# Kernel tuning notes

Hardware: AMD Instinct MI355X
Metric: run time of the kernel (lower is better)

The kernel has to match this reference:

```python
import jax, jax.numpy as jnp
import numpy as np
from jax import lax

D_MODEL, D_STATE, D_CONV, D_INNER, DT_RANK = 1024, 16, 4, 2048, 64
B_SZ, L_SEQ = 2, 4096

def setup_inputs() -> dict:
    key = jax.random.key(0)
    ks = jax.random.split(key, 12)
    s = 0.02
    x = jax.random.normal(ks[0], (B_SZ, L_SEQ, D_MODEL), jnp.float32)
    norm_w = jnp.ones((D_MODEL,), jnp.float32)
    norm_b = jnp.zeros((D_MODEL,), jnp.float32)
    W_in = jax.random.normal(ks[1], (D_MODEL, 2 * D_INNER), jnp.float32) * s
    conv_w = jax.random.normal(ks[2], (D_INNER, 1, D_CONV), jnp.float32) * 0.5
    conv_b = jnp.zeros((D_INNER,), jnp.float32)
    W_x = jax.random.normal(ks[3], (D_INNER, DT_RANK + 2 * D_STATE), jnp.float32) * s
    W_dt = jax.random.normal(ks[4], (DT_RANK, D_INNER), jnp.float32) * s
    # dt bias init as in the torch module: inverse-softplus of dt in [dt_min, dt_max]
    dt_init = jnp.exp(jax.random.uniform(ks[5], (D_INNER,)) * (np.log(0.1) - np.log(0.001)) + np.log(0.001))
    dt_init = jnp.clip(dt_init, 1e-4, None)
    b_dt = dt_init + jnp.log(-jnp.expm1(-dt_init))
    A_log = jnp.log(jnp.broadcast_to(jnp.arange(1, D_STATE + 1, dtype=jnp.float32)[None, :], (D_INNER, D_STATE)))
    D = jnp.ones((D_INNER,), jnp.float32)
    W_out = jax.random.normal(ks[6], (D_INNER, D_MODEL), jnp.float32) * s
    return {"x": x, "norm_w": norm_w, "norm_b": norm_b, "W_in": W_in,
            "conv_w": conv_w, "conv_b": conv_b, "W_x": W_x, "W_dt": W_dt,
            "b_dt": b_dt, "A_log": A_log, "D": D, "W_out": W_out}

def _silu(v):
    return v * jax.nn.sigmoid(v)

def _layernorm(v, w, b, eps=1e-5):
    mu = jnp.mean(v, axis=-1, keepdims=True)
    var = jnp.var(v, axis=-1, keepdims=True)
    return (v - mu) * lax.rsqrt(var + eps) * w + b

def _selective_scan(u, delta, A, Bm, Cm, Dp):
    # u, delta: [B,L,d_inner]; A: [d_inner,N]; Bm, Cm: [B,L,N]; Dp: [d_inner]
    Bb, L, d_inner = u.shape
    N = A.shape[1]

    def step(h, inp):
        dt_t, u_t, B_t, C_t = inp  # [B,d_inner],[B,d_inner],[B,N],[B,N]
        A_bar = jnp.exp(dt_t[..., None] * A)                       # [B,d_inner,N]
        h = A_bar * h + dt_t[..., None] * B_t[:, None, :] * u_t[..., None]
        y = jnp.sum(h * C_t[:, None, :], axis=-1)                  # [B,d_inner]
        return h, y

    h0 = jnp.zeros((Bb, d_inner, N), u.dtype)
    xs = (jnp.swapaxes(delta, 0, 1), jnp.swapaxes(u, 0, 1),
          jnp.swapaxes(Bm, 0, 1), jnp.swapaxes(Cm, 0, 1))
    _, ys = lax.scan(step, h0, xs)          # ys: [L,B,d_inner]
    y = jnp.swapaxes(ys, 0, 1)
    return y + u * Dp[None, None, :]

def reference(x, norm_w, norm_b, W_in, conv_w, conv_b, W_x, W_dt, b_dt, A_log, D, W_out):
    residual = x
    xn = _layernorm(x, norm_w, norm_b)
    xz = xn @ W_in                                      # [B,L,2*d_inner]
    x_ssm, z = jnp.split(xz, 2, axis=-1)
    # depthwise causal conv1d (torch pads both sides then truncates -> left pad)
    xt = jnp.swapaxes(x_ssm, 1, 2)                      # [B,d_inner,L]
    xt = jnp.pad(xt, ((0, 0), (0, 0), (D_CONV - 1, 0)))
    xc = lax.conv_general_dilated(xt, conv_w, window_strides=(1,), padding='VALID',
                                  feature_group_count=D_INNER,
                                  dimension_numbers=('NCH', 'OIH', 'NCH'))
    xc = xc + conv_b[None, :, None]
    x_conv = jnp.swapaxes(_silu(xc), 1, 2)              # [B,L,d_inner]
    x_dbl = x_conv @ W_x                                # [B,L,dt_rank+2N]
    dt_low, B_mat, C_mat = jnp.split(x_dbl, [DT_RANK, DT_RANK + D_STATE], axis=-1)
    delta = jax.nn.softplus(dt_low @ W_dt + b_dt)       # [B,L,d_inner]
    A = -jnp.exp(A_log)
    y = _selective_scan(x_conv, delta, A, B_mat, C_mat, D)
    y = y * _silu(z)
    return residual + y @ W_out
```

## Files before the change

### kernel.cpp

```cpp
#include <hip/hip_runtime.h>

typedef unsigned short u16;
typedef __attribute__((ext_vector_type(8))) __bf16 bf16x8;
typedef __attribute__((ext_vector_type(4))) float f32x4;

#define LSEQ 4096
#define DMODEL 1024
#define DINNER 2048

__device__ __forceinline__ float bf2f(u16 u) {
  union { unsigned u; float f; } v; v.u = ((unsigned)u) << 16; return v.f;
}
__device__ __forceinline__ u16 f2bf(float f) {
  union { float f; unsigned u; } v; v.f = f;
  unsigned r = v.u + 0x7fffu + ((v.u >> 16) & 1u);
  return (u16)(r >> 16);
}
__device__ __forceinline__ void gload_lds16(const void* g, void* l) {
  __builtin_amdgcn_global_load_lds(
      (__attribute__((address_space(1))) void*)(unsigned long long)g,
      (__attribute__((address_space(3))) void*)(unsigned int)(unsigned long long)l,
      16, 0, 0);
}
__device__ __forceinline__ float sigmoidf_(float v) { return 1.f / (1.f + __expf(-v)); }

__global__ __launch_bounds__(256) void ln_kernel(const float* __restrict__ x,
                                                 const float* __restrict__ w,
                                                 const float* __restrict__ b,
                                                 u16* __restrict__ out) {
  int row = blockIdx.x;
  const float* xr = x + (size_t)row * DMODEL;
  int t = threadIdx.x;
  float4 v = ((const float4*)xr)[t];
  float s = v.x + v.y + v.z + v.w;
  float s2 = v.x * v.x + v.y * v.y + v.z * v.z + v.w * v.w;
  for (int off = 32; off; off >>= 1) {
    s += __shfl_down(s, off);
    s2 += __shfl_down(s2, off);
  }
  __shared__ float ls[4], ls2[4];
  int wid = t >> 6;
  if ((t & 63) == 0) { ls[wid] = s; ls2[wid] = s2; }
  __syncthreads();
  s = ls[0] + ls[1] + ls[2] + ls[3];
  s2 = ls2[0] + ls2[1] + ls2[2] + ls2[3];
  float mu = s * (1.f / DMODEL);
  float var = s2 * (1.f / DMODEL) - mu * mu;
  float rs = rsqrtf(var + 1e-5f);
  float4 wv = ((const float4*)w)[t];
  float4 bv = ((const float4*)b)[t];
  unsigned p0 = (unsigned)f2bf((v.x - mu) * rs * wv.x + bv.x) |
                ((unsigned)f2bf((v.y - mu) * rs * wv.y + bv.y) << 16);
  unsigned p1 = (unsigned)f2bf((v.z - mu) * rs * wv.z + bv.z) |
                ((unsigned)f2bf((v.w - mu) * rs * wv.w + bv.w) << 16);
  ((uint2*)(out + (size_t)row * DMODEL))[t] = make_uint2(p0, p1);
}

__global__ __launch_bounds__(256) void tc_kernel(const float* __restrict__ in,
                                                 u16* __restrict__ out,
                                                 int K, int N, int Npad) {
  __shared__ float tile[32][33];
  int n0 = blockIdx.x * 32, k0 = blockIdx.y * 32;
  int tx = threadIdx.x & 31, ty = threadIdx.x >> 5;
  for (int i = ty; i < 32; i += 8) {
    int k = k0 + i, n = n0 + tx;
    tile[i][tx] = (k < K && n < N) ? in[(size_t)k * N + n] : 0.f;
  }
  __syncthreads();
  for (int i = ty; i < 32; i += 8) {
    int n = n0 + i, k = k0 + tx;
    if (n < Npad && k < K) out[(size_t)n * K + k] = f2bf(tile[tx][i]);
  }
}

__device__ __forceinline__ void stage8(const u16* grow0, int ld, int kcol0,
                                       u16* lds_u, int ln) {
  int rr = ln >> 3, kb = ln & 7;
  gload_lds16(grow0 + (size_t)rr * ld + kcol0 + ((kb ^ rr) << 3), lds_u);
}

#define LDA_FRAGS(mh, buf)                                                         \
  _Pragma("unroll") for (int mf = 0; mf < 4; ++mf)                                 \
  _Pragma("unroll") for (int kk = 0; kk < 2; ++kk)                                 \
    a[mf][kk] = *(const bf16x8*)(LA + (buf) * 16384 +                              \
        (wm * 128 + (mh) * 64 + mf * 16 + lr) * 64 + (((kk * 4 + lq) ^ key) << 3));

#define LDB_FRAGS(nh, buf)                                                         \
  _Pragma("unroll") for (int nf = 0; nf < 2; ++nf)                                 \
  _Pragma("unroll") for (int kk = 0; kk < 2; ++kk)                                 \
    bb[nh][nf][kk] = *(const bf16x8*)(LB + (buf) * 16384 +                         \
        (wn * 64 + (nh) * 32 + nf * 16 + lr) * 64 + (((kk * 4 + lq) ^ key) << 3));

#define MFMA_Q(mh, nh)                                                             \
  __builtin_amdgcn_s_setprio(1);                                                   \
  _Pragma("unroll") for (int mf = 0; mf < 4; ++mf)                                 \
  _Pragma("unroll") for (int nf = 0; nf < 2; ++nf)                                 \
  _Pragma("unroll") for (int kk = 0; kk < 2; ++kk)                                 \
    acc[(mh) * 4 + mf][(nh) * 2 + nf] = __builtin_amdgcn_mfma_f32_16x16x32_bf16(   \
        a[mf][kk], bb[nh][nf][kk], acc[(mh) * 4 + mf][(nh) * 2 + nf], 0, 0, 0);    \
  __builtin_amdgcn_s_setprio(0);

#define STAGE_A(unit, kt, buf)                                                     \
  _Pragma("unroll") for (int c = 0; c < 2; ++c) {                                  \
    int g = w * 2 + c;                                                             \
    int r0 = ((g < 8) ? g * 8 : (g - 8) * 8 + 128) + (unit) * 64;                  \
    stage8(Ag + (size_t)r0 * K, K, (kt) * 64, LA + (buf) * 16384 + r0 * 64, ln);   \
  }

#define STAGE_B(half, kt, buf)                                                     \
  _Pragma("unroll") for (int c = 0; c < 2; ++c) {                                  \
    int g = w * 2 + c;                                                             \
    int r0 = (g >> 2) * 64 + (half) * 32 + (g & 3) * 8;                            \
    stage8(Bg + (size_t)r0 * K, K, (kt) * 64, LB + (buf) * 16384 + r0 * 64, ln);   \
  }

template <int OUT_BF16, int EPI>
__global__ __launch_bounds__(512, 2) void gemm8p(const u16* __restrict__ A,
                                                 const u16* __restrict__ Bt,
                                                 void* __restrict__ Cout,
                                                 const float* __restrict__ aux,
                                                 int M, int N, int K, int cthresh) {
  __shared__ alignas(16) u16 lds[65536];
  u16* LA = lds;
  u16* LB = lds + 32768;
  int t = threadIdx.x;
  int w = t >> 6, ln = t & 63;
  int wm = w >> 2, wn = w & 3;
  int bm = blockIdx.y, bn = blockIdx.x;
  int lr = ln & 15, lq = ln >> 4, key = ln & 7;
  int NT = K >> 6;
  const u16* Ag = A + (size_t)bm * 256 * K;
  const u16* Bg = Bt + (size_t)bn * 256 * K;
  f32x4 acc[8][4] = {};
  bf16x8 a[4][2], bb[2][2][2];

  STAGE_A(0, 0, 0); STAGE_B(0, 0, 0); STAGE_B(1, 0, 0); STAGE_A(1, 0, 0);
  int k1 = NT > 1 ? 1 : 0;
  STAGE_A(0, k1, 1); STAGE_B(0, k1, 1); STAGE_B(1, k1, 1);
  asm volatile("s_waitcnt vmcnt(6)" ::: "memory");
  __builtin_amdgcn_s_barrier();

  for (int T = 0; T < NT; ++T) {
    int b0 = T & 1, b1 = b0 ^ 1;
    int kt1 = (T + 1 < NT) ? T + 1 : NT - 1;
    int kt2 = (T + 2 < NT) ? T + 2 : NT - 1;
    LDA_FRAGS(0, b0);
    LDB_FRAGS(0, b0);
    STAGE_A(1, kt1, b1);
    __builtin_amdgcn_s_barrier();
    asm volatile("s_waitcnt lgkmcnt(0)" ::: "memory");
    MFMA_Q(0, 0);
    __builtin_amdgcn_s_barrier();
    LDB_FRAGS(1, b0);
    STAGE_A(0, kt2, b0);
    __builtin_amdgcn_s_barrier();
    asm volatile("s_waitcnt lgkmcnt(0)" ::: "memory");
    MFMA_Q(0, 1);
    __builtin_amdgcn_s_barrier();
    LDA_FRAGS(1, b0);
    STAGE_B(0, kt2, b0);
    __builtin_amdgcn_s_barrier();
    asm volatile("s_waitcnt lgkmcnt(0)" ::: "memory");
    MFMA_Q(1, 1);
    __builtin_amdgcn_s_barrier();
    STAGE_B(1, kt2, b0);
    asm volatile("s_waitcnt vmcnt(6)" ::: "memory");
    __builtin_amdgcn_s_barrier();
    MFMA_Q(1, 0);
    __builtin_amdgcn_s_barrier();
  }

  int crow0 = bm * 256 + wm * 128;
  int ccol0 = bn * 256 + wn * 64;
#pragma unroll
  for (int mf = 0; mf < 8; ++mf)
#pragma unroll
    for (int nf = 0; nf < 4; ++nf)
#pragma unroll
      for (int r = 0; r < 4; ++r) {
        int row = crow0 + mf * 16 + lq * 4 + r;
        int col = ccol0 + nf * 16 + lr;
        float v = acc[mf][nf][r];
        if (EPI == 1) v += aux[(size_t)row * N + col];
        if (EPI == 2 && col >= cthresh) v = v * sigmoidf_(v);
        if (OUT_BF16)
          ((u16*)Cout)[(size_t)row * N + col] = f2bf(v);
        else
          ((float*)Cout)[(size_t)row * N + col] = v;
      }
}

template <int OUT_BF16, int EPI, int SPLITK>
__global__ __launch_bounds__(256) void gemm_bt(const u16* __restrict__ A,
                                               const u16* __restrict__ Bt,
                                               void* __restrict__ Cout,
                                               const float* __restrict__ aux,
                                               int M, int N, int K, int ld, int cthresh) {
  __shared__ alignas(16) u16 As[128 * 32];
  __shared__ alignas(16) u16 Bs[128 * 32];
  int t = threadIdx.x;
  int w = t >> 6, ln = t & 63;
  int wr = w >> 1, wc = w & 1;
  int bm = blockIdx.y, bn = blockIdx.x;
  int lr = ln & 15, lk = (ln >> 4) * 8;
  f32x4 acc[4][4] = {};
  int kz = SPLITK ? blockIdx.z * K : 0;
  const u16* Abase = A + (size_t)bm * 128 * ld + kz;
  const u16* Bbase = Bt + (size_t)bn * 128 * ld + kz;
  for (int k0 = 0; k0 < K; k0 += 32) {
#pragma unroll
    for (int c = 0; c < 2; ++c) {
      int chunk = w * 2 + c;
      int ee = chunk * 512 + ln * 8;
      int row = ee >> 5, col = ee & 31;
      gload_lds16(Abase + (size_t)row * ld + k0 + col, As + chunk * 512);
      gload_lds16(Bbase + (size_t)row * ld + k0 + col, Bs + chunk * 512);
    }
    __syncthreads();
    bf16x8 af[4], bfr[4];
#pragma unroll
    for (int m = 0; m < 4; ++m)
      af[m] = *(const bf16x8*)(As + (wr * 64 + m * 16 + lr) * 32 + lk);
#pragma unroll
    for (int n = 0; n < 4; ++n)
      bfr[n] = *(const bf16x8*)(Bs + (wc * 64 + n * 16 + lr) * 32 + lk);
#pragma unroll
    for (int m = 0; m < 4; ++m)
#pragma unroll
      for (int n = 0; n < 4; ++n)
        acc[m][n] = __builtin_amdgcn_mfma_f32_16x16x32_bf16(af[m], bfr[n], acc[m][n], 0, 0, 0);
    __syncthreads();
  }
  int rb = bm * 128 + wr * 64 + (ln >> 4) * 4;
  int cb = bn * 128 + wc * 64 + lr;
  float* Cpart = SPLITK ? ((float*)Cout + (size_t)blockIdx.z * M * N) : (float*)Cout;
#pragma unroll
  for (int m = 0; m < 4; ++m)
#pragma unroll
    for (int n = 0; n < 4; ++n)
#pragma unroll
      for (int r = 0; r < 4; ++r) {
        int row = rb + m * 16 + r;
        int col = cb + n * 16;
        float v = acc[m][n][r];
        if (EPI == 3) {
          float dtr = v + aux[col];
          v = dtr > 15.f ? dtr : __logf(1.f + __expf(dtr));
        }
        if (OUT_BF16)
          ((u16*)Cpart)[(size_t)row * N + col] = f2bf(v);
        else
          Cpart[(size_t)row * N + col] = v;
      }
}

__global__ __launch_bounds__(256) void reduce_xdbl(const float* __restrict__ part,
                                                   float* __restrict__ xdbl,
                                                   u16* __restrict__ dtlow) {
  int i = blockIdx.x * 256 + threadIdx.x;
  float s = 0.f;
#pragma unroll
  for (int z = 0; z < 8; ++z) s += part[(size_t)z * (8192 * 128) + i];
  xdbl[i] = s;
  int col = i & 127;
  if (col < 64) dtlow[(size_t)(i >> 7) * 64 + col] = f2bf(s);
}

__global__ __launch_bounds__(256) void conv_silu(const u16* __restrict__ xz,
                                                 const float* __restrict__ cw,
                                                 const float* __restrict__ cb,
                                                 u16* __restrict__ out) {
  int d = blockIdx.x * 256 + threadIdx.x;
  int l0 = blockIdx.y * 8;
  int b = blockIdx.z;
  float w0 = cw[d * 4 + 0], w1 = cw[d * 4 + 1], w2 = cw[d * 4 + 2], w3 = cw[d * 4 + 3];
  float bias = cb[d];
  const u16* xp = xz + ((size_t)b * LSEQ) * 4096 + d;
  float xv[11];
#pragma unroll
  for (int i = 0; i < 11; ++i) {
    int l = l0 - 3 + i;
    xv[i] = (l >= 0) ? bf2f(xp[(size_t)l * 4096]) : 0.f;
  }
  u16* op = out + ((size_t)b * LSEQ + l0) * DINNER + d;
#pragma unroll
  for (int i = 0; i < 8; ++i) {
    float acc = bias + w0 * xv[i] + w1 * xv[i + 1] + w2 * xv[i + 2] + w3 * xv[i + 3];
    float sv = acc * sigmoidf_(acc);
    op[(size_t)i * DINNER] = f2bf(sv);
  }
}

__device__ __forceinline__ void compute_a(float dt, const float* An, bool fast, float* av) {
  if (fast) {
    float q = __expf(-dt);
    float q2 = q * q, q4 = q2 * q2;
    av[0] = q; av[1] = q2; av[2] = q2 * q; av[3] = q4;
#pragma unroll
    for (int n = 4; n < 16; ++n) av[n] = av[n - 4] * q4;
  } else {
#pragma unroll
    for (int n = 0; n < 16; ++n) av[n] = __expf(dt * An[n]);
  }
}

__global__ __launch_bounds__(256) void scan1(const u16* __restrict__ dtbf,
                                             const u16* __restrict__ ubf,
                                             const float* __restrict__ xdbl,
                                             const float* __restrict__ A_log,
                                             float* __restrict__ P,
                                             float* __restrict__ H) {
  int d = blockIdx.x * 256 + threadIdx.x;
  int b = blockIdx.y, c = blockIdx.z;
  size_t row0 = (size_t)b * LSEQ + c * 64;
  float An[16];
  bool fast = true;
  {
    const float4* A4 = (const float4*)(A_log + (size_t)d * 16);
#pragma unroll
    for (int q = 0; q < 4; ++q) {
      float4 a = A4[q];
      An[q * 4 + 0] = -__expf(a.x);
      An[q * 4 + 1] = -__expf(a.y);
      An[q * 4 + 2] = -__expf(a.z);
      An[q * 4 + 3] = -__expf(a.w);
    }
#pragma unroll
    for (int n = 0; n < 16; ++n)
      fast = fast && (__builtin_fabsf(An[n] + (float)(n + 1)) < 1e-3f * (n + 1));
  }
  const u16* dtp = dtbf + row0 * DINNER + d;
  const u16* up = ubf + row0 * DINNER + d;
  const float* Bp = xdbl + row0 * 128 + 64;
  float h[16];
#pragma unroll
  for (int n = 0; n < 16; ++n) h[n] = 0.f;
  float sdt = 0.f;
#pragma unroll 2
  for (int i = 0; i < 64; ++i) {
    float dt = bf2f(dtp[(size_t)i * DINNER]);
    float uu = bf2f(up[(size_t)i * DINNER]);
    float dtu = dt * uu;
    sdt += dt;
    const float4* B4 = (const float4*)(Bp + (size_t)i * 128);
    float4 b0 = B4[0], b1 = B4[1], b2 = B4[2], b3 = B4[3];
    float Bf[16] = {b0.x, b0.y, b0.z, b0.w, b1.x, b1.y, b1.z, b1.w,
                    b2.x, b2.y, b2.z, b2.w, b3.x, b3.y, b3.z, b3.w};
    float av[16];
    compute_a(dt, An, fast, av);
#pragma unroll
    for (int n = 0; n < 16; ++n) h[n] = av[n] * h[n] + dtu * Bf[n];
  }
  size_t idx = (size_t)c * 65536 + ((size_t)b * DINNER + d) * 16;
  float4* P4 = (float4*)(P + idx);
  float4* H4 = (float4*)(H + idx);
#pragma unroll
  for (int q = 0; q < 4; ++q) {
    P4[q] = make_float4(__expf(An[q * 4 + 0] * sdt), __expf(An[q * 4 + 1] * sdt),
                        __expf(An[q * 4 + 2] * sdt), __expf(An[q * 4 + 3] * sdt));
    H4[q] = make_float4(h[q * 4], h[q * 4 + 1], h[q * 4 + 2], h[q * 4 + 3]);
  }
}

__global__ __launch_bounds__(256) void scan2(const float* __restrict__ P,
                                             const float* __restrict__ H,
                                             float* __restrict__ Hinit) {
  int i = blockIdx.x * 256 + threadIdx.x;
  float h = 0.f;
  for (int c = 0; c < 64; ++c) {
    Hinit[(size_t)c * 65536 + i] = h;
    h = P[(size_t)c * 65536 + i] * h + H[(size_t)c * 65536 + i];
  }
}

__global__ __launch_bounds__(256) void scan3(const u16* __restrict__ dtbf,
                                             const u16* __restrict__ ubf,
                                             const float* __restrict__ xdbl,
                                             const float* __restrict__ A_log,
                                             const float* __restrict__ Dp,
                                             const u16* __restrict__ xzbf,
                                             const float* __restrict__ Hinit,
                                             u16* __restrict__ ybf) {
  int d = blockIdx.x * 256 + threadIdx.x;
  int b = blockIdx.y, c = blockIdx.z;
  size_t row0 = (size_t)b * LSEQ + c * 64;
  float An[16];
  bool fast = true;
  {
    const float4* A4 = (const float4*)(A_log + (size_t)d * 16);
#pragma unroll
    for (int q = 0; q < 4; ++q) {
      float4 a = A4[q];
      An[q * 4 + 0] = -__expf(a.x);
      An[q * 4 + 1] = -__expf(a.y);
      An[q * 4 + 2] = -__expf(a.z);
      An[q * 4 + 3] = -__expf(a.w);
    }
#pragma unroll
    for (int n = 0; n < 16; ++n)
      fast = fast && (__builtin_fabsf(An[n] + (float)(n + 1)) < 1e-3f * (n + 1));
  }
  const u16* dtp = dtbf + row0 * DINNER + d;
  const u16* up = ubf + row0 * DINNER + d;
  const float* Bp = xdbl + row0 * 128 + 64;
  const float* Cp = xdbl + row0 * 128 + 80;
  const u16* gp = xzbf + row0 * 4096 + DINNER + d;
  u16* yp = ybf + row0 * DINNER + d;
  float Dv = Dp[d];
  float h[16];
  {
    const float4* Hi4 = (const float4*)(Hinit + (size_t)c * 65536 + ((size_t)b * DINNER + d) * 16);
#pragma unroll
    for (int q = 0; q < 4; ++q) {
      float4 hv = Hi4[q];
      h[q * 4 + 0] = hv.x; h[q * 4 + 1] = hv.y; h[q * 4 + 2] = hv.z; h[q * 4 + 3] = hv.w;
    }
  }
#pragma unroll 2
  for (int i = 0; i < 64; ++i) {
    float dt = bf2f(dtp[(size_t)i * DINNER]);
    float uu = bf2f(up[(size_t)i * DINNER]);
    float dtu = dt * uu;
    const float4* B4 = (const float4*)(Bp + (size_t)i * 128);
    float4 b0 = B4[0], b1 = B4[1], b2 = B4[2], b3 = B4[3];
    float Bf[16] = {b0.x, b0.y, b0.z, b0.w, b1.x, b1.y, b1.z, b1.w,
                    b2.x, b2.y, b2.z, b2.w, b3.x, b3.y, b3.z, b3.w};
    const float4* C4 = (const float4*)(Cp + (size_t)i * 128);
    float4 c0 = C4[0], c1 = C4[1], c2 = C4[2], c3 = C4[3];
    float Cf[16] = {c0.x, c0.y, c0.z, c0.w, c1.x, c1.y, c1.z, c1.w,
                    c2.x, c2.y, c2.z, c2.w, c3.x, c3.y, c3.z, c3.w};
    float av[16];
    compute_a(dt, An, fast, av);
    float y = 0.f;
#pragma unroll
    for (int n = 0; n < 16; ++n) {
      h[n] = av[n] * h[n] + dtu * Bf[n];
      y += h[n] * Cf[n];
    }
    float g = bf2f(gp[(size_t)i * 4096]);
    yp[(size_t)i * DINNER] = f2bf((y + uu * Dv) * g);
  }
}

extern "C" void kernel_launch(void* const* d_in, const int* in_sizes, int n_in,
                              void* d_out, int out_size, void* d_ws, size_t ws_size,
                              hipStream_t stream) {
  const float* x = (const float*)d_in[0];
  const float* nw = (const float*)d_in[1];
  const float* nb = (const float*)d_in[2];
  const float* W_in = (const float*)d_in[3];
  const float* convw = (const float*)d_in[4];
  const float* convb = (const float*)d_in[5];
  const float* W_x = (const float*)d_in[6];
  const float* W_dt = (const float*)d_in[7];
  const float* b_dt = (const float*)d_in[8];
  const float* A_log = (const float*)d_in[9];
  const float* Dp = (const float*)d_in[10];
  const float* W_out = (const float*)d_in[11];
  float* out = (float*)d_out;

  char* wp = (char*)d_ws;
  auto alloc = [&](size_t bytes) {
    char* p = wp;
    wp += (bytes + 255) & ~(size_t)255;
    return p;
  };
  u16* xz_bf = (u16*)alloc((size_t)8192 * 4096 * 2);
  u16* xconv_bf = (u16*)alloc((size_t)8192 * 2048 * 2);
  u16* xn_bf = (u16*)alloc((size_t)8192 * 1024 * 2);
  float* xdbl = (float*)alloc((size_t)8192 * 128 * 4);
  u16* dt_bf = (u16*)alloc((size_t)8192 * 2048 * 2);
  u16* dtlow_bf = (u16*)alloc((size_t)8192 * 64 * 2);
  u16* Wint = (u16*)alloc((size_t)4096 * 1024 * 2);
  u16* Wxt = (u16*)alloc((size_t)128 * 2048 * 2);
  u16* Wdtt = (u16*)alloc((size_t)2048 * 64 * 2);
  u16* Woutt = (u16*)alloc((size_t)1024 * 2048 * 2);
  float* P = (float*)alloc((size_t)64 * 65536 * 4);
  float* H = (float*)alloc((size_t)64 * 65536 * 4);
  float* Hinit = (float*)alloc((size_t)64 * 65536 * 4);
  float* xdbl_part = (float*)P;
  u16* y_bf = (u16*)P;

  tc_kernel<<<dim3(128, 32), 256, 0, stream>>>(W_in, Wint, 1024, 4096, 4096);
  tc_kernel<<<dim3(4, 64), 256, 0, stream>>>(W_x, Wxt, 2048, 96, 128);
  tc_kernel<<<dim3(64, 2), 256, 0, stream>>>(W_dt, Wdtt, 64, 2048, 2048);
  tc_kernel<<<dim3(32, 64), 256, 0, stream>>>(W_out, Woutt, 2048, 1024, 1024);

  ln_kernel<<<8192, 256, 0, stream>>>(x, nw, nb, xn_bf);
  gemm8p<1, 2><<<dim3(16, 32), 512, 0, stream>>>(xn_bf, Wint, xz_bf, nullptr,
                                                 8192, 4096, 1024, 2048);
  conv_silu<<<dim3(8, 512, 2), 256, 0, stream>>>(xz_bf, convw, convb, xconv_bf);
  gemm_bt<0, 0, 1><<<dim3(1, 64, 8), 256, 0, stream>>>(xconv_bf, Wxt, xdbl_part, nullptr,
                                                       8192, 128, 256, 2048, 0);
  reduce_xdbl<<<4096, 256, 0, stream>>>(xdbl_part, xdbl, dtlow_bf);
  gemm_bt<1, 3, 0><<<dim3(16, 64), 256, 0, stream>>>(dtlow_bf, Wdtt, dt_bf, b_dt,
                                                     8192, 2048, 64, 64, 0);
  scan1<<<dim3(8, 2, 64), 256, 0, stream>>>(dt_bf, xconv_bf, xdbl, A_log, P, H);
  scan2<<<256, 256, 0, stream>>>(P, H, Hinit);
  scan3<<<dim3(8, 2, 64), 256, 0, stream>>>(dt_bf, xconv_bf, xdbl, A_log, Dp, xz_bf,
                                            Hinit, y_bf);
  gemm8p<0, 1><<<dim3(4, 32), 512, 0, stream>>>(y_bf, Woutt, out, x,
                                                8192, 1024, 2048, 0);
}
```

Measured before the change: 346.4 us.

## Use K32 gemm with higher occupancy for in-proj and split-K out-proj

The input projection moves to a new GEMM kernel with a 32-wide K tile and half the LDS, allowing 4 blocks per CU instead of 2. Block indices are swizzled so neighbouring blocks share operand tiles in cache. The output projection, previously only 128 blocks, is split along K into two partial fp32 buffers, and a separate reduce kernel adds the partials and the residual. This targets low occupancy and poor CU fill, at the cost of extra partial-sum traffic and one more launch.

```diff
diff --git a/kernel.cpp b/kernel.cpp
--- a/kernel.cpp
+++ b/kernel.cpp
@@ -23,6 +23,14 @@
       16, 0, 0);
 }
 __device__ __forceinline__ float sigmoidf_(float v) { return 1.f / (1.f + __expf(-v)); }
+
+__device__ __forceinline__ void swz_block(int gx, int& bn, int& bm) {
+  int lin = blockIdx.x + gridDim.x * blockIdx.y;
+  int q = (gridDim.x * gridDim.y) >> 3;
+  int s = (lin & 7) * q + (lin >> 3);
+  bn = s % gx;
+  bm = s / gx;
+}
 
 __global__ __launch_bounds__(256) void ln_kernel(const float* __restrict__ x,
                                                  const float* __restrict__ w,
@@ -73,6 +81,109 @@
   }
 }
 
+__device__ __forceinline__ void stage32(const u16* gbase, int ldK, int kcol0,
+                                        u16* lds_base, int w, int ln) {
+#pragma unroll
+  for (int c = 0; c < 2; ++c) {
+    int r0 = c * 128 + w * 16;
+    int rr = ln >> 2;
+    int slog = (ln & 3) ^ (rr & 3);
+    gload_lds16(gbase + (size_t)(r0 + rr) * ldK + kcol0 + slog * 8, lds_base + r0 * 32);
+  }
+}
+
+#define LDA32(mh, buf)                                                             \
+  _Pragma("unroll") for (int mf = 0; mf < 4; ++mf)                                 \
+    a[mf] = *(const bf16x8*)(LA + (buf) * 8192 +                                   \
+        (wm * 128 + (mh) * 64 + mf * 16 + lr) * 32 + ((lq ^ (lr & 3)) << 3));
+
+#define LDB32(nh, buf, B_)                                                         \
+  _Pragma("unroll") for (int nf = 0; nf < 2; ++nf)                                 \
+    B_[nf] = *(const bf16x8*)(LB + (buf) * 8192 +                                  \
+        (wn * 64 + (nh) * 32 + nf * 16 + lr) * 32 + ((lq ^ (lr & 3)) << 3));
+
+#define MFMA_Q32(mh, nh, B_)                                                       \
+  __builtin_amdgcn_s_setprio(1);                                                   \
+  _Pragma("unroll") for (int mf = 0; mf < 4; ++mf)                                 \
+  _Pragma("unroll") for (int nf = 0; nf < 2; ++nf)                                 \
+    acc[(mh) * 4 + mf][(nh) * 2 + nf] = __builtin_amdgcn_mfma_f32_16x16x32_bf16(   \
+        a[mf], B_[nf], acc[(mh) * 4 + mf][(nh) * 2 + nf], 0, 0, 0);                \
+  __builtin_amdgcn_s_setprio(0);
+
+template <int OUT_BF16, int EPI>
+__global__ __launch_bounds__(512, 4) void gemm32(const u16* __restrict__ A,
+                                                 const u16* __restrict__ Bt,
+                                                 void* __restrict__ Cout,
+                                                 int M, int N, int K, int cthresh) {
+  __shared__ alignas(16) u16 lds[32768];
+  u16* LA = lds;
+  u16* LB = lds + 16384;
+  int t = threadIdx.x;
+  int w = t >> 6, ln = t & 63;
+  int wm = w >> 2, wn = w & 3;
+  int bn, bm;
+  swz_block(gridDim.x, bn, bm);
+  int lr = ln & 15, lq = ln >> 4;
+  int NT = K >> 5;
+  const u16* Ag = A + (size_t)bm * 256 * K;
+  const u16* Bg = Bt + (size_t)bn * 256 * K;
+  f32x4 acc[8][4] = {};
+  bf16x8 a[4], bbl[2], bbh[2];
+
+  stage32(Ag, K, 0, LA, w, ln);
+  stage32(Bg, K, 0, LB, w, ln);
+  int k1 = NT > 1 ? 1 : 0;
+  stage32(Bg, K, k1 * 32, LB + 8192, w, ln);
+  stage32(Ag, K, k1 * 32, LA + 8192, w, ln);
+  asm volatile("s_waitcnt vmcnt(4)" ::: "memory");
+  __builtin_amdgcn_s_barrier();
+
+  for (int T = 0; T < NT; ++T) {
+    int b0 = T & 1;
+    int kt2 = (T + 2 < NT) ? T + 2 : NT - 1;
+    LDA32(0, b0);
+    LDB32(0, b0, bbl);
+    __builtin_amdgcn_s_barrier();
+    asm volatile("s_waitcnt lgkmcnt(0)" ::: "memory");
+    MFMA_Q32(0, 0, bbl);
+    __builtin_amdgcn_s_barrier();
+    LDB32(1, b0, bbh);
+    __builtin_amdgcn_s_barrier();
+    asm volatile("s_waitcnt lgkmcnt(0)" ::: "memory");
+    MFMA_Q32(0, 1, bbh);
+    __builtin_amdgcn_s_barrier();
+    LDA32(1, b0);
+    stage32(Bg, K, kt2 * 32, LB + b0 * 8192, w, ln);
+    __builtin_amdgcn_s_barrier();
+    asm volatile("s_waitcnt lgkmcnt(0)" ::: "memory");
+    MFMA_Q32(1, 1, bbh);
+    __builtin_amdgcn_s_barrier();
+    stage32(Ag, K, kt2 * 32, LA + b0 * 8192, w, ln);
+    asm volatile("s_waitcnt vmcnt(4)" ::: "memory");
+    __builtin_amdgcn_s_barrier();
+    MFMA_Q32(1, 0, bbl);
+    __builtin_amdgcn_s_barrier();
+  }
+
+  int crow0 = bm * 256 + wm * 128;
+  int ccol0 = bn * 256 + wn * 64;
+#pragma unroll
+  for (int mf = 0; mf < 8; ++mf)
+#pragma unroll
+    for (int nf = 0; nf < 4; ++nf)
+#pragma unroll
+      for (int r = 0; r < 4; ++r) {
+        int row = crow0 + mf * 16 + lq * 4 + r;
+        int col = ccol0 + nf * 16 + lr;
+        float v = acc[mf][nf][r];
+        if (EPI == 2 && col >= cthresh) v = v * sigmoidf_(v);
+        if (OUT_BF16)
+          ((u16*)Cout)[(size_t)row * N + col] = f2bf(v);
+        else
+          ((float*)Cout)[(size_t)row * N + col] = v;
+      }
+}
+
 __device__ __forceinline__ void stage8(const u16* grow0, int ld, int kcol0,
                                        u16* lds_u, int ln) {
   int rr = ln >> 3, kb = ln & 7;
@@ -82,7 +193,7 @@
 #define LDA_FRAGS(mh, buf)                                                         \
   _Pragma("unroll") for (int mf = 0; mf < 4; ++mf)                                 \
   _Pragma("unroll") for (int kk = 0; kk < 2; ++kk)                                 \
-    a[mf][kk] = *(const bf16x8*)(LA + (buf) * 16384 +                              \
+    av[mf][kk] = *(const bf16x8*)(LA + (buf) * 16384 +                             \
         (wm * 128 + (mh) * 64 + mf * 16 + lr) * 64 + (((kk * 4 + lq) ^ key) << 3));
 
 #define LDB_FRAGS(nh, buf)                                                         \
@@ -97,42 +208,43 @@
   _Pragma("unroll") for (int nf = 0; nf < 2; ++nf)                                 \
   _Pragma("unroll") for (int kk = 0; kk < 2; ++kk)                                 \
     acc[(mh) * 4 + mf][(nh) * 2 + nf] = __builtin_amdgcn_mfma_f32_16x16x32_bf16(   \
-        a[mf][kk], bb[nh][nf][kk], acc[(mh) * 4 + mf][(nh) * 2 + nf], 0, 0, 0);    \
+        av[mf][kk], bb[nh][nf][kk], acc[(mh) * 4 + mf][(nh) * 2 + nf], 0, 0, 0);   \
   __builtin_amdgcn_s_setprio(0);
 
 #define STAGE_A(unit, kt, buf)                                                     \
   _Pragma("unroll") for (int c = 0; c < 2; ++c) {                                  \
     int g = w * 2 + c;                                                             \
     int r0 = ((g < 8) ? g * 8 : (g - 8) * 8 + 128) + (unit) * 64;                  \
-    stage8(Ag + (size_t)r0 * K, K, (kt) * 64, LA + (buf) * 16384 + r0 * 64, ln);   \
+    stage8(Ag + (size_t)r0 * ldK, ldK, (kt) * 64, LA + (buf) * 16384 + r0 * 64, ln); \
   }
 
 #define STAGE_B(half, kt, buf)                                                     \
   _Pragma("unroll") for (int c = 0; c < 2; ++c) {                                  \
     int g = w * 2 + c;                                                             \
     int r0 = (g >> 2) * 64 + (half) * 32 + (g & 3) * 8;                            \
-    stage8(Bg + (size_t)r0 * K, K, (kt) * 64, LB + (buf) * 16384 + r0 * 64, ln);   \
-  }
-
-template <int OUT_BF16, int EPI>
-__global__ __launch_bounds__(512, 2) void gemm8p(const u16* __restrict__ A,
-                                                 const u16* __restrict__ Bt,
-                                                 void* __restrict__ Cout,
-                                                 const float* __restrict__ aux,
-                                                 int M, int N, int K, int cthresh) {
+    stage8(Bg + (size_t)r0 * ldK, ldK, (kt) * 64, LB + (buf) * 16384 + r0 * 64, ln); \
+  }
+
+__global__ __launch_bounds__(512, 2) void gemm8p_sk(const u16* __restrict__ A,
+                                                    const u16* __restrict__ Bt,
+                                                    float* __restrict__ C0,
+                                                    float* __restrict__ C1,
+                                                    int M, int N, int Ks, int ldK) {
   __shared__ alignas(16) u16 lds[65536];
   u16* LA = lds;
   u16* LB = lds + 32768;
   int t = threadIdx.x;
   int w = t >> 6, ln = t & 63;
   int wm = w >> 2, wn = w & 3;
-  int bm = blockIdx.y, bn = blockIdx.x;
+  int bn, bm;
+  swz_block(gridDim.x, bn, bm);
   int lr = ln & 15, lq = ln >> 4, key = ln & 7;
-  int NT = K >> 6;
-  const u16* Ag = A + (size_t)bm * 256 * K;
-  const u16* Bg = Bt + (size_t)bn * 256 * K;
+  int NT = Ks >> 6;
+  int kz = blockIdx.z * Ks;
+  const u16* Ag = A + (size_t)bm * 256 * ldK + kz;
+  const u16* Bg = Bt + (size_t)bn * 256 * ldK + kz;
   f32x4 acc[8][4] = {};
-  bf16x8 a[4][2], bb[2][2][2];
+  bf16x8 av[4][2], bb[2][2][2];
 
   STAGE_A(0, 0, 0); STAGE_B(0, 0, 0); STAGE_B(1, 0, 0); STAGE_A(1, 0, 0);
   int k1 = NT > 1 ? 1 : 0;
@@ -170,6 +282,7 @@
     __builtin_amdgcn_s_barrier();
   }
 
+  float* Cpart = blockIdx.z ? C1 : C0;
   int crow0 = bm * 256 + wm * 128;
   int ccol0 = bn * 256 + wn * 64;
 #pragma unroll
@@ -180,14 +293,20 @@
       for (int r = 0; r < 4; ++r) {
         int row = crow0 + mf * 16 + lq * 4 + r;
         int col = ccol0 + nf * 16 + lr;
-        float v = acc[mf][nf][r];
-        if (EPI == 1) v += aux[(size_t)row * N + col];
-        if (EPI == 2 && col >= cthresh) v = v * sigmoidf_(v);
-        if (OUT_BF16)
-          ((u16*)Cout)[(size_t)row * N + col] = f2bf(v);
-        else
-          ((float*)Cout)[(size_t)row * N + col] = v;
+        Cpart[(size_t)row * N + col] = acc[mf][nf][r];
       }
+}
+
+__global__ __launch_bounds__(256) void reduce2(const float* __restrict__ p0,
+                                               const float* __restrict__ p1,
+                                               const float* __restrict__ x,
+                                               float* __restrict__ out) {
+  int i = blockIdx.x * 256 + threadIdx.x;
+  float4 a = ((const float4*)p0)[i];
+  float4 b = ((const float4*)p1)[i];
+  float4 c = ((const float4*)x)[i];
+  ((float4*)out)[i] = make_float4(a.x + b.x + c.x, a.y + b.y + c.y,
+                                  a.z + b.z + c.z, a.w + b.w + c.w);
 }
 
 template <int OUT_BF16, int EPI, int SPLITK>
@@ -480,6 +599,8 @@
   float* Hinit = (float*)alloc((size_t)64 * 65536 * 4);
   float* xdbl_part = (float*)P;
   u16* y_bf = (u16*)P;
+  float* gpart0 = (float*)dt_bf;
+  float* gpart1 = (float*)xconv_bf;
 
   tc_kernel<<<dim3(128, 32), 256, 0, stream>>>(W_in, Wint, 1024, 4096, 4096);
   tc_kernel<<<dim3(4, 64), 256, 0, stream>>>(W_x, Wxt, 2048, 96, 128);
@@ -487,8 +608,7 @@
   tc_kernel<<<dim3(32, 64), 256, 0, stream>>>(W_out, Woutt, 2048, 1024, 1024);
 
   ln_kernel<<<8192, 256, 0, stream>>>(x, nw, nb, xn_bf);
-  gemm8p<1, 2><<<dim3(16, 32), 512, 0, stream>>>(xn_bf, Wint, xz_bf, nullptr,
-                                                 8192, 4096, 1024, 2048);
+  gemm32<1, 2><<<dim3(16, 32), 512, 0, stream>>>(xn_bf, Wint, xz_bf, 8192, 4096, 1024, 2048);
   conv_silu<<<dim3(8, 512, 2), 256, 0, stream>>>(xz_bf, convw, convb, xconv_bf);
   gemm_bt<0, 0, 1><<<dim3(1, 64, 8), 256, 0, stream>>>(xconv_bf, Wxt, xdbl_part, nullptr,
                                                        8192, 128, 256, 2048, 0);
@@ -499,6 +619,7 @@
   scan2<<<256, 256, 0, stream>>>(P, H, Hinit);
   scan3<<<dim3(8, 2, 64), 256, 0, stream>>>(dt_bf, xconv_bf, xdbl, A_log, Dp, xz_bf,
                                             Hinit, y_bf);
-  gemm8p<0, 1><<<dim3(4, 32), 512, 0, stream>>>(y_bf, Woutt, out, x,
-                                                8192, 1024, 2048, 0);
-}
+  gemm8p_sk<<<dim3(4, 32, 2), 512, 0, stream>>>(y_bf, Woutt, gpart0, gpart1,
+                                                8192, 1024, 1024, 2048);
+  reduce2<<<8192, 256, 0, stream>>>(gpart0, gpart1, x, out);
+}
```

After: 918.5 us. 2.65x slower.

## Split-K the output projection GEMM and swizzle block order for L2 locality

Applied to the files above, without the earlier changes.

The final GEMM (8192x1024x2048) launched only 128 blocks of 256x256, which underfills the GPU. It now splits K in two, writing fp32 partials into reused scratch buffers (dt_bf, xconv_bf), then adds both partials and the residual in a separate reduce kernel. Both gemm8p kernels also remap block indices through an 8-way interleaved swizzle so concurrently running blocks share operand tiles. The split costs an extra 64 MB of partial-sum traffic and one more launch.

```diff
diff --git a/kernel.cpp b/kernel.cpp
--- a/kernel.cpp
+++ b/kernel.cpp
@@ -23,6 +23,14 @@
       16, 0, 0);
 }
 __device__ __forceinline__ float sigmoidf_(float v) { return 1.f / (1.f + __expf(-v)); }
+
+__device__ __forceinline__ void swz_block(int gx, int& bn, int& bm) {
+  int lin = blockIdx.x + gridDim.x * blockIdx.y;
+  int q = (gridDim.x * gridDim.y) >> 3;
+  int s = (lin & 7) * q + (lin >> 3);
+  bn = s % gx;
+  bm = s / gx;
+}
 
 __global__ __launch_bounds__(256) void ln_kernel(const float* __restrict__ x,
                                                  const float* __restrict__ w,
@@ -82,7 +90,7 @@
 #define LDA_FRAGS(mh, buf)                                                         \
   _Pragma("unroll") for (int mf = 0; mf < 4; ++mf)                                 \
   _Pragma("unroll") for (int kk = 0; kk < 2; ++kk)                                 \
-    a[mf][kk] = *(const bf16x8*)(LA + (buf) * 16384 +                              \
+    av[mf][kk] = *(const bf16x8*)(LA + (buf) * 16384 +                             \
         (wm * 128 + (mh) * 64 + mf * 16 + lr) * 64 + (((kk * 4 + lq) ^ key) << 3));
 
 #define LDB_FRAGS(nh, buf)                                                         \
@@ -97,21 +105,57 @@
   _Pragma("unroll") for (int nf = 0; nf < 2; ++nf)                                 \
   _Pragma("unroll") for (int kk = 0; kk < 2; ++kk)                                 \
     acc[(mh) * 4 + mf][(nh) * 2 + nf] = __builtin_amdgcn_mfma_f32_16x16x32_bf16(   \
-        a[mf][kk], bb[nh][nf][kk], acc[(mh) * 4 + mf][(nh) * 2 + nf], 0, 0, 0);    \
+        av[mf][kk], bb[nh][nf][kk], acc[(mh) * 4 + mf][(nh) * 2 + nf], 0, 0, 0);   \
   __builtin_amdgcn_s_setprio(0);
 
 #define STAGE_A(unit, kt, buf)                                                     \
   _Pragma("unroll") for (int c = 0; c < 2; ++c) {                                  \
     int g = w * 2 + c;                                                             \
     int r0 = ((g < 8) ? g * 8 : (g - 8) * 8 + 128) + (unit) * 64;                  \
-    stage8(Ag + (size_t)r0 * K, K, (kt) * 64, LA + (buf) * 16384 + r0 * 64, ln);   \
+    stage8(Ag + (size_t)r0 * ldK, ldK, (kt) * 64, LA + (buf) * 16384 + r0 * 64, ln); \
   }
 
 #define STAGE_B(half, kt, buf)                                                     \
   _Pragma("unroll") for (int c = 0; c < 2; ++c) {                                  \
     int g = w * 2 + c;                                                             \
     int r0 = (g >> 2) * 64 + (half) * 32 + (g & 3) * 8;                            \
-    stage8(Bg + (size_t)r0 * K, K, (kt) * 64, LB + (buf) * 16384 + r0 * 64, ln);   \
+    stage8(Bg + (size_t)r0 * ldK, ldK, (kt) * 64, LB + (buf) * 16384 + r0 * 64, ln); \
+  }
+
+#define GEMM8P_BODY                                                                \
+  STAGE_A(0, 0, 0); STAGE_B(0, 0, 0); STAGE_B(1, 0, 0); STAGE_A(1, 0, 0);          \
+  int k1 = NT > 1 ? 1 : 0;                                                         \
+  STAGE_A(0, k1, 1); STAGE_B(0, k1, 1); STAGE_B(1, k1, 1);                         \
+  asm volatile("s_waitcnt vmcnt(6)" ::: "memory");                                 \
+  __builtin_amdgcn_s_barrier();                                                    \
+  for (int T = 0; T < NT; ++T) {                                                   \
+    int b0 = T & 1, b1 = b0 ^ 1;                                                   \
+    int kt1 = (T + 1 < NT) ? T + 1 : NT - 1;                                       \
+    int kt2 = (T + 2 < NT) ? T + 2 : NT - 1;                                       \
+    LDA_FRAGS(0, b0);                                                              \
+    LDB_FRAGS(0, b0);                                                              \
+    STAGE_A(1, kt1, b1);                                                           \
+    __builtin_amdgcn_s_barrier();                                                  \
+    asm volatile("s_waitcnt lgkmcnt(0)" ::: "memory");                             \
+    MFMA_Q(0, 0);                                                                  \
+    __builtin_amdgcn_s_barrier();                                                  \
+    LDB_FRAGS(1, b0);                                                              \
+    STAGE_A(0, kt2, b0);                                                           \
+    __builtin_amdgcn_s_barrier();                                                  \
+    asm volatile("s_waitcnt lgkmcnt(0)" ::: "memory");                             \
+    MFMA_Q(0, 1);                                                                  \
+    __builtin_amdgcn_s_barrier();                                                  \
+    LDA_FRAGS(1, b0);                                                              \
+    STAGE_B(0, kt2, b0);                                                           \
+    __builtin_amdgcn_s_barrier();                                                  \
+    asm volatile("s_waitcnt lgkmcnt(0)" ::: "memory");                             \
+    MFMA_Q(1, 1);                                                                  \
+    __builtin_amdgcn_s_barrier();                                                  \
+    STAGE_B(1, kt2, b0);                                                           \
+    asm volatile("s_waitcnt vmcnt(6)" ::: "memory");                               \
+    __builtin_amdgcn_s_barrier();                                                  \
+    MFMA_Q(1, 0);                                                                  \
+    __builtin_amdgcn_s_barrier();                                                  \
   }
 
 template <int OUT_BF16, int EPI>
@@ -126,49 +170,17 @@
   int t = threadIdx.x;
   int w = t >> 6, ln = t & 63;
   int wm = w >> 2, wn = w & 3;
-  int bm = blockIdx.y, bn = blockIdx.x;
+  int bn, bm;
+  swz_block(gridDim.x, bn, bm);
   int lr = ln & 15, lq = ln >> 4, key = ln & 7;
+  int ldK = K;
   int NT = K >> 6;
-  const u16* Ag = A + (size_t)bm * 256 * K;
-  const u16* Bg = Bt + (size_t)bn * 256 * K;
+  const u16* Ag = A + (size_t)bm * 256 * ldK;
+  const u16* Bg = Bt + (size_t)bn * 256 * ldK;
   f32x4 acc[8][4] = {};
-  bf16x8 a[4][2], bb[2][2][2];
-
-  STAGE_A(0, 0, 0); STAGE_B(0, 0, 0); STAGE_B(1, 0, 0); STAGE_A(1, 0, 0);
-  int k1 = NT > 1 ? 1 : 0;
-  STAGE_A(0, k1, 1); STAGE_B(0, k1, 1); STAGE_B(1, k1, 1);
-  asm volatile("s_waitcnt vmcnt(6)" ::: "memory");
-  __builtin_amdgcn_s_barrier();
-
-  for (int T = 0; T < NT; ++T) {
-    int b0 = T & 1, b1 = b0 ^ 1;
-    int kt1 = (T + 1 < NT) ? T + 1 : NT - 1;
-    int kt2 = (T + 2 < NT) ? T + 2 : NT - 1;
-    LDA_FRAGS(0, b0);
-    LDB_FRAGS(0, b0);
-    STAGE_A(1, kt1, b1);
-    __builtin_amdgcn_s_barrier();
-    asm volatile("s_waitcnt lgkmcnt(0)" ::: "memory");
-    MFMA_Q(0, 0);
-    __builtin_amdgcn_s_barrier();
-    LDB_FRAGS(1, b0);
-    STAGE_A(0, kt2, b0);
-    __builtin_amdgcn_s_barrier();
-    asm volatile("s_waitcnt lgkmcnt(0)" ::: "memory");
-    MFMA_Q(0, 1);
-    __builtin_amdgcn_s_barrier();
-    LDA_FRAGS(1, b0);
-    STAGE_B(0, kt2, b0);
-    __builtin_amdgcn_s_barrier();
-    asm volatile("s_waitcnt lgkmcnt(0)" ::: "memory");
-    MFMA_Q(1, 1);
-    __builtin_amdgcn_s_barrier();
-    STAGE_B(1, kt2, b0);
-    asm volatile("s_waitcnt vmcnt(6)" ::: "memory");
-    __builtin_amdgcn_s_barrier();
-    MFMA_Q(1, 0);
-    __builtin_amdgcn_s_barrier();
-  }
+  bf16x8 av[4][2], bb[2][2][2];
+
+  GEMM8P_BODY
 
   int crow0 = bm * 256 + wm * 128;
   int ccol0 = bn * 256 + wn * 64;
@@ -188,6 +200,56 @@
         else
           ((float*)Cout)[(size_t)row * N + col] = v;
       }
+}
+
+__global__ __launch_bounds__(512, 2) void gemm8p_sk(const u16* __restrict__ A,
+                                                    const u16* __restrict__ Bt,
+                                                    float* __restrict__ C0,
+                                                    float* __restrict__ C1,
+                                                    int M, int N, int Ks, int ldK) {
+  __shared__ alignas(16) u16 lds[65536];
+  u16* LA = lds;
+  u16* LB = lds + 32768;
+  int t = threadIdx.x;
+  int w = t >> 6, ln = t & 63;
+  int wm = w >> 2, wn = w & 3;
+  int bn, bm;
+  swz_block(gridDim.x, bn, bm);
+  int lr = ln & 15, lq = ln >> 4, key = ln & 7;
+  int NT = Ks >> 6;
+  int kz = blockIdx.z * Ks;
+  const u16* Ag = A + (size_t)bm * 256 * ldK + kz;
+  const u16* Bg = Bt + (size_t)bn * 256 * ldK + kz;
+  f32x4 acc[8][4] = {};
+  bf16x8 av[4][2], bb[2][2][2];
+
+  GEMM8P_BODY
+
+  float* Cpart = blockIdx.z ? C1 : C0;
+  int crow0 = bm * 256 + wm * 128;
+  int ccol0 = bn * 256 + wn * 64;
+#pragma unroll
+  for (int mf = 0; mf < 8; ++mf)
+#pragma unroll
+    for (int nf = 0; nf < 4; ++nf)
+#pragma unroll
+      for (int r = 0; r < 4; ++r) {
+        int row = crow0 + mf * 16 + lq * 4 + r;
+        int col = ccol0 + nf * 16 + lr;
+        Cpart[(size_t)row * N + col] = acc[mf][nf][r];
+      }
+}
+
+__global__ __launch_bounds__(256) void reduce2(const float* __restrict__ p0,
+                                               const float* __restrict__ p1,
+                                               const float* __restrict__ x,
+                                               float* __restrict__ out) {
+  int i = blockIdx.x * 256 + threadIdx.x;
+  float4 a = ((const float4*)p0)[i];
+  float4 b = ((const float4*)p1)[i];
+  float4 c = ((const float4*)x)[i];
+  ((float4*)out)[i] = make_float4(a.x + b.x + c.x, a.y + b.y + c.y,
+                                  a.z + b.z + c.z, a.w + b.w + c.w);
 }
 
 template <int OUT_BF16, int EPI, int SPLITK>
@@ -480,6 +542,8 @@
   float* Hinit = (float*)alloc((size_t)64 * 65536 * 4);
   float* xdbl_part = (float*)P;
   u16* y_bf = (u16*)P;
+  float* gpart0 = (float*)dt_bf;
+  float* gpart1 = (float*)xconv_bf;
 
   tc_kernel<<<dim3(128, 32), 256, 0, stream>>>(W_in, Wint, 1024, 4096, 4096);
   tc_kernel<<<dim3(4, 64), 256, 0, stream>>>(W_x, Wxt, 2048, 96, 128);
@@ -499,6 +563,7 @@
   scan2<<<256, 256, 0, stream>>>(P, H, Hinit);
   scan3<<<dim3(8, 2, 64), 256, 0, stream>>>(dt_bf, xconv_bf, xdbl, A_log, Dp, xz_bf,
                                             Hinit, y_bf);
-  gemm8p<0, 1><<<dim3(4, 32), 512, 0, stream>>>(y_bf, Woutt, out, x,
-                                                8192, 1024, 2048, 0);
-}
+  gemm8p_sk<<<dim3(4, 32, 2), 512, 0, stream>>>(y_bf, Woutt, gpart0, gpart1,
+                                                8192, 1024, 1024, 2048);
+  reduce2<<<8192, 256, 0, stream>>>(gpart0, gpart1, x, out);
+}
```

After: 331.0 us. -4.4%, faster.

## Use 128x256 tiles for output GEMM and swizzle block order

Applied to the files above, without the earlier changes.

Adds a gemm128_res kernel with a 128-row by 256-column tile for the final y@W_out plus residual GEMM. This doubles the grid from 128 to 256 blocks so more CUs are occupied. It also adds an XCD-aware block-index swizzle to both GEMM kernels so that neighbouring tiles share L2. The trade-off is lower arithmetic intensity per block and a reworked pipelined staging schedule.

```diff
diff --git a/kernel.cpp b/kernel.cpp
--- a/kernel.cpp
+++ b/kernel.cpp
@@ -23,6 +23,14 @@
       16, 0, 0);
 }
 __device__ __forceinline__ float sigmoidf_(float v) { return 1.f / (1.f + __expf(-v)); }
+
+__device__ __forceinline__ void swz_block(int gx, int& bn, int& bm) {
+  int lin = blockIdx.x + gridDim.x * blockIdx.y;
+  int q = (gridDim.x * gridDim.y) >> 3;
+  int s = (lin & 7) * q + (lin >> 3);
+  bn = s % gx;
+  bm = s / gx;
+}
 
 __global__ __launch_bounds__(256) void ln_kernel(const float* __restrict__ x,
                                                  const float* __restrict__ w,
@@ -82,7 +90,7 @@
 #define LDA_FRAGS(mh, buf)                                                         \
   _Pragma("unroll") for (int mf = 0; mf < 4; ++mf)                                 \
   _Pragma("unroll") for (int kk = 0; kk < 2; ++kk)                                 \
-    a[mf][kk] = *(const bf16x8*)(LA + (buf) * 16384 +                              \
+    av[mf][kk] = *(const bf16x8*)(LA + (buf) * 16384 +                             \
         (wm * 128 + (mh) * 64 + mf * 16 + lr) * 64 + (((kk * 4 + lq) ^ key) << 3));
 
 #define LDB_FRAGS(nh, buf)                                                         \
@@ -97,21 +105,21 @@
   _Pragma("unroll") for (int nf = 0; nf < 2; ++nf)                                 \
   _Pragma("unroll") for (int kk = 0; kk < 2; ++kk)                                 \
     acc[(mh) * 4 + mf][(nh) * 2 + nf] = __builtin_amdgcn_mfma_f32_16x16x32_bf16(   \
-        a[mf][kk], bb[nh][nf][kk], acc[(mh) * 4 + mf][(nh) * 2 + nf], 0, 0, 0);    \
+        av[mf][kk], bb[nh][nf][kk], acc[(mh) * 4 + mf][(nh) * 2 + nf], 0, 0, 0);   \
   __builtin_amdgcn_s_setprio(0);
 
 #define STAGE_A(unit, kt, buf)                                                     \
   _Pragma("unroll") for (int c = 0; c < 2; ++c) {                                  \
     int g = w * 2 + c;                                                             \
     int r0 = ((g < 8) ? g * 8 : (g - 8) * 8 + 128) + (unit) * 64;                  \
-    stage8(Ag + (size_t)r0 * K, K, (kt) * 64, LA + (buf) * 16384 + r0 * 64, ln);   \
+    stage8(Ag + (size_t)r0 * ldK, ldK, (kt) * 64, LA + (buf) * 16384 + r0 * 64, ln); \
   }
 
 #define STAGE_B(half, kt, buf)                                                     \
   _Pragma("unroll") for (int c = 0; c < 2; ++c) {                                  \
     int g = w * 2 + c;                                                             \
     int r0 = (g >> 2) * 64 + (half) * 32 + (g & 3) * 8;                            \
-    stage8(Bg + (size_t)r0 * K, K, (kt) * 64, LB + (buf) * 16384 + r0 * 64, ln);   \
+    stage8(Bg + (size_t)r0 * ldK, ldK, (kt) * 64, LB + (buf) * 16384 + r0 * 64, ln); \
   }
 
 template <int OUT_BF16, int EPI>
@@ -126,13 +134,15 @@
   int t = threadIdx.x;
   int w = t >> 6, ln = t & 63;
   int wm = w >> 2, wn = w & 3;
-  int bm = blockIdx.y, bn = blockIdx.x;
+  int bn, bm;
+  swz_block(gridDim.x, bn, bm);
   int lr = ln & 15, lq = ln >> 4, key = ln & 7;
+  int ldK = K;
   int NT = K >> 6;
-  const u16* Ag = A + (size_t)bm * 256 * K;
-  const u16* Bg = Bt + (size_t)bn * 256 * K;
+  const u16* Ag = A + (size_t)bm * 256 * ldK;
+  const u16* Bg = Bt + (size_t)bn * 256 * ldK;
   f32x4 acc[8][4] = {};
-  bf16x8 a[4][2], bb[2][2][2];
+  bf16x8 av[4][2], bb[2][2][2];
 
   STAGE_A(0, 0, 0); STAGE_B(0, 0, 0); STAGE_B(1, 0, 0); STAGE_A(1, 0, 0);
   int k1 = NT > 1 ? 1 : 0;
@@ -187,6 +197,111 @@
           ((u16*)Cout)[(size_t)row * N + col] = f2bf(v);
         else
           ((float*)Cout)[(size_t)row * N + col] = v;
+      }
+}
+
+#define LDA128(mh, buf)                                                            \
+  _Pragma("unroll") for (int mf2 = 0; mf2 < 2; ++mf2)                              \
+  _Pragma("unroll") for (int kk = 0; kk < 2; ++kk)                                 \
+    av[mf2][kk] = *(const bf16x8*)(LA + (buf) * 8192 +                             \
+        (wm * 64 + (mh) * 32 + mf2 * 16 + lr) * 64 + (((kk * 4 + lq) ^ key) << 3));
+
+#define LDB128(nh, buf, B_)                                                        \
+  _Pragma("unroll") for (int nf2 = 0; nf2 < 2; ++nf2)                              \
+  _Pragma("unroll") for (int kk = 0; kk < 2; ++kk)                                 \
+    B_[nf2][kk] = *(const bf16x8*)(LB + (buf) * 16384 +                            \
+        (wn * 64 + (nh) * 32 + nf2 * 16 + lr) * 64 + (((kk * 4 + lq) ^ key) << 3));
+
+#define MFMA_Q128(mh, nh, B_)                                                      \
+  __builtin_amdgcn_s_setprio(1);                                                   \
+  _Pragma("unroll") for (int mf2 = 0; mf2 < 2; ++mf2)                              \
+  _Pragma("unroll") for (int nf2 = 0; nf2 < 2; ++nf2)                              \
+  _Pragma("unroll") for (int kk = 0; kk < 2; ++kk)                                 \
+    acc[(mh) * 2 + mf2][(nh) * 2 + nf2] = __builtin_amdgcn_mfma_f32_16x16x32_bf16( \
+        av[mf2][kk], B_[nf2][kk], acc[(mh) * 2 + mf2][(nh) * 2 + nf2], 0, 0, 0);   \
+  __builtin_amdgcn_s_setprio(0);
+
+#define STAGE_A128(unit, kt, buf)                                                  \
+  {                                                                                \
+    int r0 = (w >> 2) * 64 + (unit) * 32 + (w & 3) * 8;                            \
+    stage8(Ag + (size_t)r0 * ldK, ldK, (kt) * 64, LA + (buf) * 8192 + r0 * 64, ln); \
+  }
+
+#define STAGE_B128(half, kt, buf)                                                  \
+  _Pragma("unroll") for (int c = 0; c < 2; ++c) {                                  \
+    int g = w * 2 + c;                                                             \
+    int r0 = (g >> 2) * 64 + (half) * 32 + (g & 3) * 8;                            \
+    stage8(Bg + (size_t)r0 * ldK, ldK, (kt) * 64, LB + (buf) * 16384 + r0 * 64, ln); \
+  }
+
+__global__ __launch_bounds__(512, 2) void gemm128_res(const u16* __restrict__ A,
+                                                      const u16* __restrict__ Bt,
+                                                      float* __restrict__ Cout,
+                                                      const float* __restrict__ res,
+                                                      int M, int N, int K) {
+  __shared__ alignas(16) u16 lds[49152];
+  u16* LA = lds;
+  u16* LB = lds + 16384;
+  int t = threadIdx.x;
+  int w = t >> 6, ln = t & 63;
+  int wm = w >> 2, wn = w & 3;
+  int bn, bm;
+  swz_block(gridDim.x, bn, bm);
+  int lr = ln & 15, lq = ln >> 4, key = ln & 7;
+  int ldK = K;
+  int NT = K >> 6;
+  const u16* Ag = A + (size_t)bm * 128 * ldK;
+  const u16* Bg = Bt + (size_t)bn * 256 * ldK;
+  f32x4 acc[4][4] = {};
+  bf16x8 av[2][2], bbl[2][2], bbh[2][2];
+
+  STAGE_A128(0, 0, 0); STAGE_B128(0, 0, 0); STAGE_B128(1, 0, 0); STAGE_A128(1, 0, 0);
+  int k1 = NT > 1 ? 1 : 0;
+  STAGE_A128(0, k1, 1); STAGE_B128(0, k1, 1); STAGE_B128(1, k1, 1);
+  asm volatile("s_waitcnt vmcnt(5)" ::: "memory");
+  __builtin_amdgcn_s_barrier();
+
+  for (int T = 0; T < NT; ++T) {
+    int b0 = T & 1, b1 = b0 ^ 1;
+    int kt1 = (T + 1 < NT) ? T + 1 : NT - 1;
+    int kt2 = (T + 2 < NT) ? T + 2 : NT - 1;
+    LDA128(0, b0);
+    LDB128(0, b0, bbl);
+    STAGE_A128(1, kt1, b1);
+    __builtin_amdgcn_s_barrier();
+    asm volatile("s_waitcnt lgkmcnt(0)" ::: "memory");
+    MFMA_Q128(0, 0, bbl);
+    __builtin_amdgcn_s_barrier();
+    LDB128(1, b0, bbh);
+    STAGE_A128(0, kt2, b0);
+    __builtin_amdgcn_s_barrier();
+    asm volatile("s_waitcnt lgkmcnt(0)" ::: "memory");
+    MFMA_Q128(0, 1, bbh);
+    __builtin_amdgcn_s_barrier();
+    LDA128(1, b0);
+    STAGE_B128(0, kt2, b0);
+    __builtin_amdgcn_s_barrier();
+    asm volatile("s_waitcnt lgkmcnt(0)" ::: "memory");
+    MFMA_Q128(1, 1, bbh);
+    __builtin_amdgcn_s_barrier();
+    STAGE_B128(1, kt2, b0);
+    asm volatile("s_waitcnt vmcnt(5)" ::: "memory");
+    __builtin_amdgcn_s_barrier();
+    MFMA_Q128(1, 0, bbl);
+    __builtin_amdgcn_s_barrier();
+  }
+
+  int crow0 = bm * 128 + wm * 64;
+  int ccol0 = bn * 256 + wn * 64;
+#pragma unroll
+  for (int mf = 0; mf < 4; ++mf)
+#pragma unroll
+    for (int nf = 0; nf < 4; ++nf)
+#pragma unroll
+      for (int r = 0; r < 4; ++r) {
+        int row = crow0 + mf * 16 + lq * 4 + r;
+        int col = ccol0 + nf * 16 + lr;
+        Cout[(size_t)row * N + col] = acc[mf][nf][r] + res[(size_t)row * N + col];
       }
 }
 
@@ -499,6 +614,5 @@
   scan2<<<256, 256, 0, stream>>>(P, H, Hinit);
   scan3<<<dim3(8, 2, 64), 256, 0, stream>>>(dt_bf, xconv_bf, xdbl, A_log, Dp, xz_bf,
                                             Hinit, y_bf);
-  gemm8p<0, 1><<<dim3(4, 32), 512, 0, stream>>>(y_bf, Woutt, out, x,
-                                                8192, 1024, 2048, 0);
-}
+  gemm128_res<<<dim3(4, 64), 512, 0, stream>>>(y_bf, Woutt, out, x, 8192, 1024, 2048);
+}
```

After: 317.4 us. 8.4% less time.
